# Kernel optimization log

Measured on AMD Instinct MI355X. Metric: run time of the kernel, lower is better.

## Reference

```python
import jax, jax.numpy as jnp
import numpy as np

EPS = 1e-8

def _gn1(x, w, b):
    # GroupNorm(num_groups=1): normalize each sample over (C, T), per-channel affine.
    mean = jnp.mean(x, axis=(1, 2), keepdims=True)
    var = jnp.mean((x - mean) ** 2, axis=(1, 2), keepdims=True)
    xn = (x - mean) * jax.lax.rsqrt(var + EPS)
    return xn * w[None, :, None] + b[None, :, None]

def _film(h, e, gw, gb, bw, bb):
    # gamma/beta: Linear -> ReLU (dropout is identity in eval), broadcast over time.
    gamma = jax.nn.relu(e @ gw.T + gb)  # [B, C]
    beta = jax.nn.relu(e @ bw.T + bb)   # [B, C]
    return gamma[:, :, None] * h + beta[:, :, None]

def setup_inputs() -> dict:
    key = jax.random.key(0)
    ks = jax.random.split(key, 16)
    B, C, T = 16, 256, 16000
    s = lambda k, shape, scale: jax.random.normal(k, shape, dtype=jnp.float32) * scale
    return {
        "x": s(ks[0], (B, C, T), 1.0),
        "cue": s(ks[1], (B, 512), 1.0),
        "gn_a_w": jnp.ones((C,), jnp.float32), "gn_a_b": jnp.zeros((C,), jnp.float32),
        "gn_n_w": jnp.ones((C,), jnp.float32), "gn_n_b": jnp.zeros((C,), jnp.float32),
        "f1g_w": s(ks[2], (C, 512), 0.04), "f1g_b": jnp.zeros((C,), jnp.float32),
        "f1b_w": s(ks[3], (C, 512), 0.04), "f1b_b": jnp.zeros((C,), jnp.float32),
        "ln1_w": jnp.ones((C,), jnp.float32), "ln1_b": jnp.zeros((C,), jnp.float32),
        "conv1_w": s(ks[4], (128, C), 0.06),
        "cds_w": s(ks[5], (256, 512), 0.04),
        "f2g_w": s(ks[6], (128, 256), 0.06), "f2g_b": jnp.zeros((128,), jnp.float32),
        "f2b_w": s(ks[7], (128, 256), 0.06), "f2b_b": jnp.zeros((128,), jnp.float32),
        "ln2_w": jnp.ones((128,), jnp.float32), "ln2_b": jnp.zeros((128,), jnp.float32),
        "conv2_w": s(ks[8], (256, 128), 0.08),
    }

def reference(x, cue, gn_a_w, gn_a_b, gn_n_w, gn_n_b, f1g_w, f1g_b, f1b_w, f1b_b,
              ln1_w, ln1_b, conv1_w, cds_w, f2g_w, f2g_b, f2b_w, f2b_b,
              ln2_w, ln2_b, conv2_w):
    x = _gn1(x, gn_a_w, gn_a_b)                 # norm_audio (GroupNorm(1, C))
    x = _gn1(x, gn_n_w, gn_n_b)                 # norm (GroupNorm(1, C))
    x = _film(x, cue, f1g_w, f1g_b, f1b_w, f1b_b) + x  # film1 + residual
    x = _gn1(x, ln1_w, ln1_b)                   # layer_norm1
    x = jnp.einsum('bct,oc->bot', x, conv1_w)   # 1x1 Conv1d, no bias -> [B,128,T]
    cue2 = jax.nn.relu(cue @ cds_w.T)           # cue_down_sample2 -> [B,256]
    x = _film(x, cue2, f2g_w, f2g_b, f2b_w, f2b_b) + x  # film2 + residual
    x = _gn1(x, ln2_w, ln2_b)                   # layer_norm2
    x = jnp.einsum('bct,oc->bot', x, conv2_w)   # 1x1 Conv1d -> [B,256,T]
    return x
```

## Files before the change

kernel.cpp:

```cpp
#include <hip/hip_runtime.h>
#include <hip/hip_bf16.h>
#include <hip/hip_fp16.h>

#define T_LEN   16000
#define NB      16
#define NTT     250
#define NTB     125
#define EPSV    1e-8f

typedef _Float16 f16x8 __attribute__((ext_vector_type(8)));
typedef float    f32x4 __attribute__((ext_vector_type(4)));

__device__ __forceinline__ ushort f2h(float f) {
    _Float16 h = (_Float16)f;
    return *(ushort*)&h;
}
__device__ __forceinline__ float f4c(const float4& v, int i) {
    return i == 0 ? v.x : i == 1 ? v.y : i == 2 ? v.z : v.w;
}
__device__ __forceinline__ void gld16(const ushort* g, ushort* l) {
    __builtin_amdgcn_global_load_lds(
        (const __attribute__((address_space(1))) uint*)g,
        (__attribute__((address_space(3))) uint*)l, 16, 0, 0);
}
__device__ __forceinline__ float waveRed64(float v) {
    #pragma unroll
    for (int m = 1; m <= 32; m <<= 1) v += __shfl_xor(v, m, 64);
    return v;
}
__device__ __forceinline__ float4 ntload4(const float* p) {
    f32x4 v = __builtin_nontemporal_load((const f32x4*)p);
    return make_float4(v[0], v[1], v[2], v[3]);
}

__global__ __launch_bounds__(256) void kP1F(
    const float* __restrict__ x, ushort* __restrict__ Xp,
    float* __restrict__ sp, float* __restrict__ qp,
    const float* __restrict__ cue,
    const float* __restrict__ f1g_w, const float* __restrict__ f1g_b,
    const float* __restrict__ f1b_w, const float* __restrict__ f1b_b,
    const float* __restrict__ cds_w,
    float* __restrict__ G1, float* __restrict__ B1, float* __restrict__ CUE2)
{
    const int bid = blockIdx.x;
    if (bid < 256) {
        const int c = bid;
        const int lane = threadIdx.x & 63, w = threadIdx.x >> 6;
        const float4 wg0 = *(const float4*)(f1g_w + c*512 + lane*8);
        const float4 wg1 = *(const float4*)(f1g_w + c*512 + lane*8 + 4);
        const float4 wb0 = *(const float4*)(f1b_w + c*512 + lane*8);
        const float4 wb1 = *(const float4*)(f1b_w + c*512 + lane*8 + 4);
        const float4 wc0 = *(const float4*)(cds_w + c*512 + lane*8);
        const float4 wc1 = *(const float4*)(cds_w + c*512 + lane*8 + 4);
        #pragma unroll
        for (int bb = 0; bb < 4; ++bb) {
            const int b = w*4 + bb;
            const float4 u0 = *(const float4*)(cue + b*512 + lane*8);
            const float4 u1 = *(const float4*)(cue + b*512 + lane*8 + 4);
            float g = 0.f, bt = 0.f, cv = 0.f;
            #pragma unroll
            for (int i = 0; i < 4; ++i) {
                g  = fmaf(f4c(u0,i), f4c(wg0,i), g);  g  = fmaf(f4c(u1,i), f4c(wg1,i), g);
                bt = fmaf(f4c(u0,i), f4c(wb0,i), bt); bt = fmaf(f4c(u1,i), f4c(wb1,i), bt);
                cv = fmaf(f4c(u0,i), f4c(wc0,i), cv); cv = fmaf(f4c(u1,i), f4c(wc1,i), cv);
            }
            g = waveRed64(g); bt = waveRed64(bt); cv = waveRed64(cv);
            if (lane == 0) {
                G1[b*256 + c]   = fmaxf(g + f1g_b[c], 0.f) + 1.f;
                B1[b*256 + c]   = fmaxf(bt + f1b_b[c], 0.f);
                CUE2[b*256 + c] = fmaxf(cv, 0.f);
            }
        }
        return;
    }

    const int pb = bid - 256;
    const int b = pb / NTT, tt = pb % NTT;
    const int t0 = tt * 64;
    const int tid = threadIdx.x;
    const int cq = tid >> 2, jq = tid & 3;
    __shared__ __align__(16) ushort Hs[256][68];

    #pragma unroll
    for (int cc = 0; cc < 4; ++cc) {
        const int c = cc*64 + cq;
        float s4 = 0.f, q4 = 0.f;
        #pragma unroll
        for (int i = 0; i < 4; ++i) {
            const int ts = (jq + i*4)*4;
            const float4 v = ntload4(x + ((size_t)(b*256 + c))*T_LEN + t0 + ts);
            s4 += v.x + v.y + v.z + v.w;
            q4 += v.x*v.x + v.y*v.y + v.z*v.z + v.w*v.w;
            const ushort h0 = f2h(v.x), h1 = f2h(v.y), h2 = f2h(v.z), h3 = f2h(v.w);
            uint2 pk;
            pk.x = (uint)h0 | ((uint)h1 << 16);
            pk.y = (uint)h2 | ((uint)h3 << 16);
            *(uint2*)&Hs[c][ts] = pk;
        }
        s4 += __shfl_xor(s4, 1, 4); s4 += __shfl_xor(s4, 2, 4);
        q4 += __shfl_xor(q4, 1, 4); q4 += __shfl_xor(q4, 2, 4);
        if (jq == 0) {
            sp[((size_t)b*NTT + tt)*256 + c] = s4;
            qp[((size_t)b*NTT + tt)*256 + c] = q4;
        }
    }
    __syncthreads();
    ushort* dst = Xp + ((size_t)(b*NTT + tt)*4)*4096;
    #pragma unroll
    for (int k = 0; k < 8; ++k) {
        const int d  = tid + k*256;
        const int kc = d >> 9, r = d & 511;
        const int t  = r >> 3, us = r & 7;
        const int u  = us ^ (t & 7);
        const int c0 = kc*64 + u*8;
        uint4 val;
        val.x = (uint)Hs[c0+0][t] | ((uint)Hs[c0+1][t] << 16);
        val.y = (uint)Hs[c0+2][t] | ((uint)Hs[c0+3][t] << 16);
        val.z = (uint)Hs[c0+4][t] | ((uint)Hs[c0+5][t] << 16);
        val.w = (uint)Hs[c0+6][t] | ((uint)Hs[c0+7][t] << 16);
        *(uint4*)(dst + (size_t)d*8) = val;
    }
}

__global__ __launch_bounds__(256) void kR_reduce(
    const float* __restrict__ sp, const float* __restrict__ qp,
    float* __restrict__ s1, float* __restrict__ q1)
{
    const int cg = blockIdx.x, b = blockIdx.y;
    const int ci = threadIdx.x & 31, ig = threadIdx.x >> 5;
    const int c = cg*32 + ci;
    float s = 0.f, q = 0.f;
    for (int i = ig; i < NTT; i += 8) {
        s += sp[((size_t)b*NTT + i)*256 + c];
        q += qp[((size_t)b*NTT + i)*256 + c];
    }
    __shared__ float rs[8][32], rq[8][32];
    rs[ig][ci] = s; rq[ig][ci] = q;
    __syncthreads();
    if (threadIdx.x < 32) {
        float ss = 0.f, qq = 0.f;
        #pragma unroll
        for (int g = 0; g < 8; ++g) { ss += rs[g][threadIdx.x]; qq += rq[g][threadIdx.x]; }
        s1[b*256 + cg*32 + threadIdx.x] = ss;
        q1[b*256 + cg*32 + threadIdx.x] = qq;
    }
}

__device__ __forceinline__ float blockSum256(float v, float* red)
{
    #pragma unroll
    for (int off = 32; off; off >>= 1) v += __shfl_down(v, off, 64);
    __syncthreads();
    if ((threadIdx.x & 63) == 0) red[threadIdx.x >> 6] = v;
    __syncthreads();
    return red[0] + red[1] + red[2] + red[3];
}

__global__ __launch_bounds__(256) void kBM_stats(
    const float* __restrict__ s1, const float* __restrict__ q1,
    const float* __restrict__ gn_a_w, const float* __restrict__ gn_a_b,
    const float* __restrict__ gn_n_w, const float* __restrict__ gn_n_b,
    const float* __restrict__ G1, const float* __restrict__ B1,
    const float* __restrict__ ln1_w, const float* __restrict__ ln1_b,
    float* __restrict__ a4o, float* __restrict__ d4o)
{
    const int b = blockIdx.x;
    const int c = threadIdx.x;
    __shared__ float red[4];

    const float sc = s1[b*256 + c];
    const float qc = q1[b*256 + c];

    const float Ninv = 1.f / (256.f * 16000.f);
    const float Tf = 16000.f;

    float S  = blockSum256(sc, red);
    float Q  = blockSum256(qc, red);
    float mu1 = S * Ninv;
    float var1 = Q * Ninv - mu1 * mu1;
    float r1 = rsqrtf(var1 + EPSV);
    float a1 = gn_a_w[c] * r1;
    float d1 = gn_a_b[c] - mu1 * r1 * gn_a_w[c];

    float S2 = blockSum256(a1*sc + Tf*d1, red);
    float Q2 = blockSum256(a1*a1*qc + 2.f*a1*d1*sc + Tf*d1*d1, red);
    float mu2 = S2 * Ninv;
    float var2 = Q2 * Ninv - mu2 * mu2;
    float r2 = rsqrtf(var2 + EPSV);
    float wn = gn_n_w[c];
    float a2 = wn * r2 * a1;
    float d2 = wn * r2 * (d1 - mu2) + gn_n_b[c];

    const float g1 = G1[b*256 + c];
    const float b1 = B1[b*256 + c];
    float a3 = g1 * a2;
    float d3 = g1 * d2 + b1;

    float S3 = blockSum256(a3*sc + Tf*d3, red);
    float Q3 = blockSum256(a3*a3*qc + 2.f*a3*d3*sc + Tf*d3*d3, red);
    float mu3 = S3 * Ninv;
    float var3 = Q3 * Ninv - mu3 * mu3;
    float r3 = rsqrtf(var3 + EPSV);
    float w1 = ln1_w[c];
    a4o[b*256 + c] = w1 * r3 * a3;
    d4o[b*256 + c] = w1 * r3 * (d3 - mu3) + ln1_b[c];
}

__global__ __launch_bounds__(256) void kM2(
    const float* __restrict__ CUE2,
    const float* __restrict__ f2g_w, const float* __restrict__ f2g_b,
    const float* __restrict__ f2b_w, const float* __restrict__ f2b_b,
    const float* __restrict__ conv1_w,
    const float* __restrict__ a4, const float* __restrict__ d4,
    float* __restrict__ G2, float* __restrict__ E, ushort* __restrict__ Msf)
{
    const int og = blockIdx.x, b = blockIdx.y;
    const int tid = threadIdx.x;
    __shared__ float sc2[256], sa4[256], sd4[256], sg2[16];
    sc2[tid] = CUE2[b*256 + tid];
    sa4[tid] = a4[b*256 + tid];
    sd4[tid] = d4[b*256 + tid];
    __syncthreads();

    const int oi = tid >> 4, l16 = tid & 15;
    const int o = og*16 + oi;
    float g = 0.f, bt = 0.f, ed = 0.f;
    #pragma unroll
    for (int q = 0; q < 4; ++q) {
        const int k0 = l16*16 + q*4;
        const float4 a  = *(const float4*)(f2g_w  + o*256 + k0);
        const float4 bb = *(const float4*)(f2b_w  + o*256 + k0);
        const float4 c  = *(const float4*)(conv1_w + o*256 + k0);
        const float4 u  = *(const float4*)(&sc2[k0]);
        const float4 dd = *(const float4*)(&sd4[k0]);
        #pragma unroll
        for (int i = 0; i < 4; ++i) {
            g  = fmaf(f4c(u,i),  f4c(a,i),  g);
            bt = fmaf(f4c(u,i),  f4c(bb,i), bt);
            ed = fmaf(f4c(dd,i), f4c(c,i),  ed);
        }
    }
    #pragma unroll
    for (int m = 1; m <= 8; m <<= 1) {
        g  += __shfl_xor(g, m, 16);
        bt += __shfl_xor(bt, m, 16);
        ed += __shfl_xor(ed, m, 16);
    }
    if (l16 == 0) {
        const float G2v = fmaxf(g + f2g_b[o], 0.f) + 1.f;
        const float B2v = fmaxf(bt + f2b_b[o], 0.f);
        G2[b*128 + o] = G2v;
        E[b*128 + o]  = G2v * ed + B2v;
        sg2[oi] = G2v;
    }
    __syncthreads();
    const float av = sa4[tid];
    #pragma unroll
    for (int i = 0; i < 16; ++i) {
        const int oo = og*16 + i;
        Msf[((size_t)b*128 + oo)*256 + tid] = f2h(sg2[i] * conv1_w[oo*256 + tid] * av);
    }
}

__global__ __launch_bounds__(256) void kC_gemm(
    const ushort* __restrict__ Xp, const ushort* __restrict__ Msf,
    const float* __restrict__ E,
    float* __restrict__ q2p)
{
    const int tb = blockIdx.x, b = blockIdx.y;
    const int tid = threadIdx.x, lane = tid & 63, w = tid >> 6;
    const int wo = w >> 1, wt = w & 1;
    const int sub = lane >> 4, li = lane & 15;
    const int o0 = wo * 64;
    __shared__ __align__(16) ushort Bs[32768];
    __shared__ float sQp[2][128];

    const ushort* src = Xp + ((size_t)(b*NTT + 2*tb)*4)*4096;
    const ushort* mp  = Msf + (size_t)b*128*256;

    f32x4 acc[4][4];
    #pragma unroll
    for (int i = 0; i < 4; ++i)
        #pragma unroll
        for (int jx = 0; jx < 4; ++jx) acc[i][jx] = (f32x4){0.f,0.f,0.f,0.f};

    #pragma unroll
    for (int m = 0; m < 16; ++m) {
        const int off = m*2048 + w*512;
        gld16(src + off + lane*8, &Bs[off]);
    }
    __syncthreads();

    #pragma unroll
    for (int ks = 0; ks < 8; ++ks) {
        const int kc = ks >> 1;
        const int uo = (ks & 1)*4 + sub;
        f16x8 xf[4];
        #pragma unroll
        for (int ft = 0; ft < 4; ++ft) {
            const int tl = ft*16 + li;
            xf[ft] = *(const f16x8*)&Bs[(wt*4 + kc)*4096 + tl*64 + (uo ^ (tl & 7))*8];
        }
        const int k8 = kc*64 + (ks & 1)*32 + 8*sub;
        #pragma unroll
        for (int fo = 0; fo < 4; ++fo) {
            const f16x8 mf = *(const f16x8*)(mp + (size_t)(o0 + fo*16 + li)*256 + k8);
            #pragma unroll
            for (int ft = 0; ft < 4; ++ft)
                acc[ft][fo] = __builtin_amdgcn_mfma_f32_16x16x32_f16(xf[ft], mf, acc[ft][fo], 0, 0, 0);
        }
    }

    #pragma unroll
    for (int fo = 0; fo < 4; ++fo) {
        const int o = o0 + fo*16 + li;
        const float ev = E[b*128 + o];
        float qv = 0.f;
        #pragma unroll
        for (int ft = 0; ft < 4; ++ft)
            #pragma unroll
            for (int r = 0; r < 4; ++r) {
                const float z = acc[ft][fo][r] + ev;
                qv += z*z;
            }
        qv += __shfl_xor(qv, 16, 64); qv += __shfl_xor(qv, 32, 64);
        if (sub == 0) sQp[wt][o] = qv;
    }
    __syncthreads();
    if (tid < 128)
        q2p[((size_t)b*NTB + tb)*128 + tid] = sQp[0][tid] + sQp[1][tid];
}

__global__ __launch_bounds__(256) void kD2_buildF(
    const float* __restrict__ q2p,
    const float* __restrict__ ln2_w, const float* __restrict__ ln2_b,
    const float* __restrict__ Ev,
    const float* __restrict__ a4, const float* __restrict__ G2,
    const float* __restrict__ s1,
    const float* __restrict__ conv1_w, const float* __restrict__ conv2_w,
    ushort* __restrict__ Fsf, float* __restrict__ h)
{
    const int b = blockIdx.y, pg = blockIdx.x;
    const int tid = threadIdx.x;
    __shared__ float Qs[32][128];
    __shared__ float sA2[128], sAE[128], sAS[256];
    __shared__ float rS[2], rQ[2];

    sAS[tid] = a4[b*256 + tid] * s1[b*256 + tid];
    __syncthreads();

    float s2v = 0.f, qq = 0.f;
    if (tid < 128) {
        float dot = 0.f;
        #pragma unroll 4
        for (int c4 = 0; c4 < 64; ++c4) {
            const float4 cw = *(const float4*)(conv1_w + tid*256 + c4*4);
            const float4 as = *(const float4*)(&sAS[c4*4]);
            dot = fmaf(cw.x, as.x, dot); dot = fmaf(cw.y, as.y, dot);
            dot = fmaf(cw.z, as.z, dot); dot = fmaf(cw.w, as.w, dot);
        }
        s2v = G2[b*128 + tid] * dot + 16000.f * Ev[b*128 + tid];
        for (int tb = 0; tb < NTB; ++tb)
            qq += q2p[((size_t)b*NTB + tb)*128 + tid];
        float S = s2v, Q = qq;
        #pragma unroll
        for (int off = 32; off; off >>= 1) {
            S += __shfl_down(S, off, 64);
            Q += __shfl_down(Q, off, 64);
        }
        if ((tid & 63) == 0) { rS[tid >> 6] = S; rQ[tid >> 6] = Q; }
    }
    __syncthreads();
    const float N2inv = 1.f / (128.f * 16000.f);
    const float mu  = (rS[0] + rS[1]) * N2inv;
    const float var = (rQ[0] + rQ[1]) * N2inv - mu * mu;
    const float r = rsqrtf(var + EPSV);
    if (tid < 128) {
        const float a2v = ln2_w[tid] * r;
        const float d2v = ln2_b[tid] - mu * ln2_w[tid] * r;
        sA2[tid] = a2v;
        sAE[tid] = a2v * Ev[b*128 + tid] + d2v;
    }
    __syncthreads();

    #pragma unroll
    for (int k = 0; k < 16; ++k) {
        const int idx = tid + k*256;
        const int p = idx >> 7, o = idx & 127;
        Qs[p][o] = conv2_w[(pg*32 + p)*128 + o] * sA2[o] * G2[b*128 + o];
    }
    __syncthreads();
    float acc[32];
    #pragma unroll
    for (int p = 0; p < 32; ++p) acc[p] = 0.f;
    for (int o = 0; o < 128; ++o) {
        const float mv = conv1_w[o*256 + tid];
        #pragma unroll
        for (int p = 0; p < 32; ++p) acc[p] = fmaf(Qs[p][o], mv, acc[p]);
    }
    const float a = a4[b*256 + tid];
    #pragma unroll
    for (int p = 0; p < 32; ++p) {
        const size_t idx = ((size_t)b*256 + pg*32 + p)*256 + tid;
        Fsf[idx] = f2h(acc[p] * a);
    }
    if (tid < 32) {
        const int p = pg*32 + tid;
        float hv = 0.f;
        for (int o = 0; o < 128; ++o)
            hv += conv2_w[p*128 + o] * sAE[o];
        h[b*256 + p] = hv;
    }
}

__global__ __launch_bounds__(256) void kE_gemm(
    const ushort* __restrict__ Xp, const ushort* __restrict__ Fsf,
    const float* __restrict__ h, float* __restrict__ out)
{
    const int tt = blockIdx.x;
    const int b = blockIdx.y >> 1;
    const int o_base = (blockIdx.y & 1) * 128;
    const int tid = threadIdx.x, lane = tid & 63, w = tid >> 6;
    const int sub = lane >> 4, li = lane & 15;
    const int o0 = o_base + w * 32, t0 = tt * 64;
    __shared__ __align__(16) ushort Bs[16384];

    const ushort* src = Xp + ((size_t)(b*NTT + tt)*4)*4096;
    const ushort* fp  = Fsf + (size_t)b*65536;

    f32x4 acc[4][2];
    #pragma unroll
    for (int i = 0; i < 4; ++i)
        #pragma unroll
        for (int jx = 0; jx < 2; ++jx) acc[i][jx] = (f32x4){0.f,0.f,0.f,0.f};

    #pragma unroll
    for (int m = 0; m < 8; ++m) {
        const int off = m*2048 + w*512;
        gld16(src + off + lane*8, &Bs[off]);
    }
    __syncthreads();

    #pragma unroll
    for (int ks = 0; ks < 8; ++ks) {
        const int kc = ks >> 1;
        const int uo = (ks & 1)*4 + sub;
        f16x8 xf[4];
        #pragma unroll
        for (int ft = 0; ft < 4; ++ft) {
            const int tl = ft*16 + li;
            xf[ft] = *(const f16x8*)&Bs[kc*4096 + tl*64 + (uo ^ (tl & 7))*8];
        }
        const int k8 = kc*64 + (ks & 1)*32 + 8*sub;
        #pragma unroll
        for (int fo = 0; fo < 2; ++fo) {
            const f16x8 ff = *(const f16x8*)(fp + (size_t)(o0 + fo*16 + li)*256 + k8);
            #pragma unroll
            for (int ft = 0; ft < 4; ++ft)
                acc[ft][fo] = __builtin_amdgcn_mfma_f32_16x16x32_f16(xf[ft], ff, acc[ft][fo], 0, 0, 0);
        }
    }

    #pragma unroll
    for (int fo = 0; fo < 2; ++fo) {
        const int o = o0 + fo*16 + li;
        const float hv = h[b*256 + o];
        float* obase = out + ((size_t)(b*256 + o))*T_LEN + t0;
        #pragma unroll
        for (int ft = 0; ft < 4; ++ft) {
            f32x4 v;
            v[0] = acc[ft][fo][0] + hv;
            v[1] = acc[ft][fo][1] + hv;
            v[2] = acc[ft][fo][2] + hv;
            v[3] = acc[ft][fo][3] + hv;
            __builtin_nontemporal_store(v, (f32x4*)(obase + ft*16 + sub*4));
        }
    }
}

extern "C" void kernel_launch(void* const* d_in, const int* in_sizes, int n_in,
                              void* d_out, int out_size, void* d_ws, size_t ws_size,
                              hipStream_t stream)
{
    const float* x       = (const float*)d_in[0];
    const float* cue     = (const float*)d_in[1];
    const float* gn_a_w  = (const float*)d_in[2];
    const float* gn_a_b  = (const float*)d_in[3];
    const float* gn_n_w  = (const float*)d_in[4];
    const float* gn_n_b  = (const float*)d_in[5];
    const float* f1g_w   = (const float*)d_in[6];
    const float* f1g_b   = (const float*)d_in[7];
    const float* f1b_w   = (const float*)d_in[8];
    const float* f1b_b   = (const float*)d_in[9];
    const float* ln1_w   = (const float*)d_in[10];
    const float* ln1_b   = (const float*)d_in[11];
    const float* conv1_w = (const float*)d_in[12];
    const float* cds_w   = (const float*)d_in[13];
    const float* f2g_w   = (const float*)d_in[14];
    const float* f2g_b   = (const float*)d_in[15];
    const float* f2b_w   = (const float*)d_in[16];
    const float* f2b_b   = (const float*)d_in[17];
    const float* ln2_w   = (const float*)d_in[18];
    const float* ln2_b   = (const float*)d_in[19];
    const float* conv2_w = (const float*)d_in[20];
    float* out = (float*)d_out;

    float* ws = (float*)d_ws;
    float*  sp   = ws;
    float*  qp   = ws + 1024000;
    float*  G1   = ws + 2048000;
    float*  B1   = ws + 2052096;
    float*  CUE2 = ws + 2056192;
    float*  G2   = ws + 2060288;
    float*  a4   = ws + 2062336;
    float*  d4   = ws + 2066432;
    float*  E    = ws + 2070528;
    float*  h    = ws + 2072576;
    float*  s1   = ws + 2076672;
    float*  q1   = ws + 2080768;
    float*  q2p  = ws + 2084864;
    ushort* Msf  = (ushort*)(ws + 2340864);
    ushort* Fsf  = (ushort*)(ws + 2603008);
    ushort* Xp   = (ushort*)(ws + 3127296);

    kP1F<<<256 + NTT*NB, 256, 0, stream>>>(x, Xp, sp, qp,
        cue, f1g_w, f1g_b, f1b_w, f1b_b, cds_w, G1, B1, CUE2);

    kR_reduce<<<dim3(8, NB), 256, 0, stream>>>(sp, qp, s1, q1);

    kBM_stats<<<NB, 256, 0, stream>>>(s1, q1, gn_a_w, gn_a_b, gn_n_w, gn_n_b,
                                      G1, B1, ln1_w, ln1_b, a4, d4);

    kM2<<<dim3(8, NB), 256, 0, stream>>>(CUE2, f2g_w, f2g_b, f2b_w, f2b_b,
                                         conv1_w, a4, d4, G2, E, Msf);

    kC_gemm<<<dim3(NTB, NB), 256, 0, stream>>>(Xp, Msf, E, q2p);

    kD2_buildF<<<dim3(8, NB), 256, 0, stream>>>(q2p, ln2_w, ln2_b, E,
                                                a4, G2, s1, conv1_w, conv2_w,
                                                Fsf, h);

    kE_gemm<<<dim3(NTT, NB*2), 256, 0, stream>>>(Xp, Fsf, h, out);
}
```

Measured before the change: 306.5 us.

## Fuse partial-stat reduction and GroupNorm stats into P1 via last-block atomic counters

Removes the separate kR_reduce and kBM_stats launches. Each time-tile block of kP1F increments a per-batch atomic counter, and the last block for each batch waits for the FiLM blocks to finish through a global counter. That block then reduces the partial sums and computes the normalization coefficients inline. This saves two kernel launches and their tail gaps, but adds a memset, a spin-wait, and a serial 250-step reduction done by a single block per batch.

```diff
diff --git a/kernel.cpp b/kernel.cpp
--- a/kernel.cpp
+++ b/kernel.cpp
@@ -31,6 +31,16 @@
 __device__ __forceinline__ float4 ntload4(const float* p) {
     f32x4 v = __builtin_nontemporal_load((const f32x4*)p);
     return make_float4(v[0], v[1], v[2], v[3]);
+}
+
+__device__ __forceinline__ float blockSum256(float v, float* red)
+{
+    #pragma unroll
+    for (int off = 32; off; off >>= 1) v += __shfl_down(v, off, 64);
+    __syncthreads();
+    if ((threadIdx.x & 63) == 0) red[threadIdx.x >> 6] = v;
+    __syncthreads();
+    return red[0] + red[1] + red[2] + red[3];
 }
 
 __global__ __launch_bounds__(256) void kP1F(
@@ -40,12 +50,19 @@
     const float* __restrict__ f1g_w, const float* __restrict__ f1g_b,
     const float* __restrict__ f1b_w, const float* __restrict__ f1b_b,
     const float* __restrict__ cds_w,
-    float* __restrict__ G1, float* __restrict__ B1, float* __restrict__ CUE2)
+    float* __restrict__ G1, float* __restrict__ B1, float* __restrict__ CUE2,
+    int* __restrict__ cnt,
+    const float* __restrict__ gn_a_w, const float* __restrict__ gn_a_b,
+    const float* __restrict__ gn_n_w, const float* __restrict__ gn_n_b,
+    const float* __restrict__ ln1_w,  const float* __restrict__ ln1_b,
+    float* __restrict__ s1, float* __restrict__ a4o, float* __restrict__ d4o)
 {
     const int bid = blockIdx.x;
+    const int tid = threadIdx.x;
+
     if (bid < 256) {
         const int c = bid;
-        const int lane = threadIdx.x & 63, w = threadIdx.x >> 6;
+        const int lane = tid & 63, w = tid >> 6;
         const float4 wg0 = *(const float4*)(f1g_w + c*512 + lane*8);
         const float4 wg1 = *(const float4*)(f1g_w + c*512 + lane*8 + 4);
         const float4 wb0 = *(const float4*)(f1b_w + c*512 + lane*8);
@@ -71,15 +88,19 @@
                 CUE2[b*256 + c] = fmaxf(cv, 0.f);
             }
         }
+        __threadfence();
+        __syncthreads();
+        if (tid == 0) atomicAdd(&cnt[0], 1);
         return;
     }
 
     const int pb = bid - 256;
     const int b = pb / NTT, tt = pb % NTT;
     const int t0 = tt * 64;
-    const int tid = threadIdx.x;
     const int cq = tid >> 2, jq = tid & 3;
     __shared__ __align__(16) ushort Hs[256][68];
+    __shared__ float red[4];
+    __shared__ int isw;
 
     #pragma unroll
     for (int cc = 0; cc < 4; ++cc) {
@@ -120,56 +141,29 @@
         val.w = (uint)Hs[c0+6][t] | ((uint)Hs[c0+7][t] << 16);
         *(uint4*)(dst + (size_t)d*8) = val;
     }
-}
-
-__global__ __launch_bounds__(256) void kR_reduce(
-    const float* __restrict__ sp, const float* __restrict__ qp,
-    float* __restrict__ s1, float* __restrict__ q1)
-{
-    const int cg = blockIdx.x, b = blockIdx.y;
-    const int ci = threadIdx.x & 31, ig = threadIdx.x >> 5;
-    const int c = cg*32 + ci;
-    float s = 0.f, q = 0.f;
-    for (int i = ig; i < NTT; i += 8) {
-        s += sp[((size_t)b*NTT + i)*256 + c];
-        q += qp[((size_t)b*NTT + i)*256 + c];
-    }
-    __shared__ float rs[8][32], rq[8][32];
-    rs[ig][ci] = s; rq[ig][ci] = q;
-    __syncthreads();
-    if (threadIdx.x < 32) {
-        float ss = 0.f, qq = 0.f;
-        #pragma unroll
-        for (int g = 0; g < 8; ++g) { ss += rs[g][threadIdx.x]; qq += rq[g][threadIdx.x]; }
-        s1[b*256 + cg*32 + threadIdx.x] = ss;
-        q1[b*256 + cg*32 + threadIdx.x] = qq;
-    }
-}
-
-__device__ __forceinline__ float blockSum256(float v, float* red)
-{
-    #pragma unroll
-    for (int off = 32; off; off >>= 1) v += __shfl_down(v, off, 64);
-    __syncthreads();
-    if ((threadIdx.x & 63) == 0) red[threadIdx.x >> 6] = v;
-    __syncthreads();
-    return red[0] + red[1] + red[2] + red[3];
-}
-
-__global__ __launch_bounds__(256) void kBM_stats(
-    const float* __restrict__ s1, const float* __restrict__ q1,
-    const float* __restrict__ gn_a_w, const float* __restrict__ gn_a_b,
-    const float* __restrict__ gn_n_w, const float* __restrict__ gn_n_b,
-    const float* __restrict__ G1, const float* __restrict__ B1,
-    const float* __restrict__ ln1_w, const float* __restrict__ ln1_b,
-    float* __restrict__ a4o, float* __restrict__ d4o)
-{
-    const int b = blockIdx.x;
-    const int c = threadIdx.x;
-    __shared__ float red[4];
-
-    const float sc = s1[b*256 + c];
-    const float qc = q1[b*256 + c];
+
+    __threadfence();
+    __syncthreads();
+    if (tid == 0) {
+        const int old = atomicAdd(&cnt[1 + b], 1);
+        isw = (old == NTT - 1) ? 1 : 0;
+    }
+    __syncthreads();
+    if (!isw) return;
+
+    if (tid == 0) {
+        while (atomicAdd(&cnt[0], 0) < 256) { }
+    }
+    __syncthreads();
+    __threadfence();
+
+    const int c = tid;
+    float sc = 0.f, qc = 0.f;
+    for (int i = 0; i < NTT; ++i) {
+        sc += sp[((size_t)b*NTT + i)*256 + c];
+        qc += qp[((size_t)b*NTT + i)*256 + c];
+    }
+    s1[b*256 + c] = sc;
 
     const float Ninv = 1.f / (256.f * 16000.f);
     const float Tf = 16000.f;
@@ -517,19 +511,18 @@
     float*  E    = ws + 2070528;
     float*  h    = ws + 2072576;
     float*  s1   = ws + 2076672;
-    float*  q1   = ws + 2080768;
-    float*  q2p  = ws + 2084864;
-    ushort* Msf  = (ushort*)(ws + 2340864);
-    ushort* Fsf  = (ushort*)(ws + 2603008);
-    ushort* Xp   = (ushort*)(ws + 3127296);
+    float*  q2p  = ws + 2080768;
+    int*    cnt  = (int*)(ws + 2336768);
+    ushort* Msf  = (ushort*)(ws + 2336800);
+    ushort* Fsf  = (ushort*)(ws + 2598944);
+    ushort* Xp   = (ushort*)(ws + 3123232);
+
+    hipMemsetAsync(cnt, 0, 128, stream);
 
     kP1F<<<256 + NTT*NB, 256, 0, stream>>>(x, Xp, sp, qp,
-        cue, f1g_w, f1g_b, f1b_w, f1b_b, cds_w, G1, B1, CUE2);
-
-    kR_reduce<<<dim3(8, NB), 256, 0, stream>>>(sp, qp, s1, q1);
-
-    kBM_stats<<<NB, 256, 0, stream>>>(s1, q1, gn_a_w, gn_a_b, gn_n_w, gn_n_b,
-                                      G1, B1, ln1_w, ln1_b, a4, d4);
+        cue, f1g_w, f1g_b, f1b_w, f1b_b, cds_w, G1, B1, CUE2,
+        cnt, gn_a_w, gn_a_b, gn_n_w, gn_n_b, ln1_w, ln1_b,
+        s1, a4, d4);
 
     kM2<<<dim3(8, NB), 256, 0, stream>>>(CUE2, f2g_w, f2g_b, f2b_w, f2b_b,
                                          conv1_w, a4, d4, G2, E, Msf);
```

Measured after the change: 1.108 ms. 262% more time.

## Fuse stats kernel into kM2 and double-buffer two time tiles in kE_gemm

Applied to the files above, without the earlier changes.

Merges the per-batch GroupNorm stats kernel into the FiLM2/Msf builder, so each of the 8 blocks per batch recomputes the stats redundantly and one launch plus the d4 round trip go away. kE_gemm now processes two 64-sample time tiles per block: the F weight fragments are loaded into registers once, and the second X tile is prefetched into a second LDS buffer while the first is computed. This halves the grid and reuses weight loads, at the cost of more registers and LDS per block, which may lower occupancy.

```diff
diff --git a/kernel.cpp b/kernel.cpp
--- a/kernel.cpp
+++ b/kernel.cpp
@@ -31,6 +31,16 @@
 __device__ __forceinline__ float4 ntload4(const float* p) {
     f32x4 v = __builtin_nontemporal_load((const f32x4*)p);
     return make_float4(v[0], v[1], v[2], v[3]);
+}
+
+__device__ __forceinline__ float blockSum256(float v, float* red)
+{
+    #pragma unroll
+    for (int off = 32; off; off >>= 1) v += __shfl_down(v, off, 64);
+    __syncthreads();
+    if ((threadIdx.x & 63) == 0) red[threadIdx.x >> 6] = v;
+    __syncthreads();
+    return red[0] + red[1] + red[2] + red[3];
 }
 
 __global__ __launch_bounds__(256) void kP1F(
@@ -146,27 +156,23 @@
     }
 }
 
-__device__ __forceinline__ float blockSum256(float v, float* red)
-{
-    #pragma unroll
-    for (int off = 32; off; off >>= 1) v += __shfl_down(v, off, 64);
-    __syncthreads();
-    if ((threadIdx.x & 63) == 0) red[threadIdx.x >> 6] = v;
-    __syncthreads();
-    return red[0] + red[1] + red[2] + red[3];
-}
-
-__global__ __launch_bounds__(256) void kBM_stats(
+__global__ __launch_bounds__(256) void kM2F(
     const float* __restrict__ s1, const float* __restrict__ q1,
     const float* __restrict__ gn_a_w, const float* __restrict__ gn_a_b,
     const float* __restrict__ gn_n_w, const float* __restrict__ gn_n_b,
     const float* __restrict__ G1, const float* __restrict__ B1,
     const float* __restrict__ ln1_w, const float* __restrict__ ln1_b,
-    float* __restrict__ a4o, float* __restrict__ d4o)
-{
-    const int b = blockIdx.x;
+    const float* __restrict__ CUE2,
+    const float* __restrict__ f2g_w, const float* __restrict__ f2g_b,
+    const float* __restrict__ f2b_w, const float* __restrict__ f2b_b,
+    const float* __restrict__ conv1_w,
+    float* __restrict__ a4o, float* __restrict__ G2,
+    float* __restrict__ E, ushort* __restrict__ Msf)
+{
+    const int og = blockIdx.x, b = blockIdx.y;
     const int c = threadIdx.x;
     __shared__ float red[4];
+    __shared__ float sc2[256], sa4[256], sd4[256], sg2[16];
 
     const float sc = s1[b*256 + c];
     const float qc = q1[b*256 + c];
@@ -191,10 +197,10 @@
     float a2 = wn * r2 * a1;
     float d2 = wn * r2 * (d1 - mu2) + gn_n_b[c];
 
-    const float g1 = G1[b*256 + c];
-    const float b1 = B1[b*256 + c];
-    float a3 = g1 * a2;
-    float d3 = g1 * d2 + b1;
+    const float g1v = G1[b*256 + c];
+    const float b1v = B1[b*256 + c];
+    float a3 = g1v * a2;
+    float d3 = g1v * d2 + b1v;
 
     float S3 = blockSum256(a3*sc + Tf*d3, red);
     float Q3 = blockSum256(a3*a3*qc + 2.f*a3*d3*sc + Tf*d3*d3, red);
@@ -202,27 +208,15 @@
     float var3 = Q3 * Ninv - mu3 * mu3;
     float r3 = rsqrtf(var3 + EPSV);
     float w1 = ln1_w[c];
-    a4o[b*256 + c] = w1 * r3 * a3;
-    d4o[b*256 + c] = w1 * r3 * (d3 - mu3) + ln1_b[c];
-}
-
-__global__ __launch_bounds__(256) void kM2(
-    const float* __restrict__ CUE2,
-    const float* __restrict__ f2g_w, const float* __restrict__ f2g_b,
-    const float* __restrict__ f2b_w, const float* __restrict__ f2b_b,
-    const float* __restrict__ conv1_w,
-    const float* __restrict__ a4, const float* __restrict__ d4,
-    float* __restrict__ G2, float* __restrict__ E, ushort* __restrict__ Msf)
-{
-    const int og = blockIdx.x, b = blockIdx.y;
-    const int tid = threadIdx.x;
-    __shared__ float sc2[256], sa4[256], sd4[256], sg2[16];
-    sc2[tid] = CUE2[b*256 + tid];
-    sa4[tid] = a4[b*256 + tid];
-    sd4[tid] = d4[b*256 + tid];
-    __syncthreads();
-
-    const int oi = tid >> 4, l16 = tid & 15;
+    const float a4v = w1 * r3 * a3;
+    const float d4v = w1 * r3 * (d3 - mu3) + ln1_b[c];
+    sa4[c] = a4v;
+    sd4[c] = d4v;
+    if (og == 0) a4o[b*256 + c] = a4v;
+    sc2[c] = CUE2[b*256 + c];
+    __syncthreads();
+
+    const int oi = c >> 4, l16 = c & 15;
     const int o = og*16 + oi;
     float g = 0.f, bt = 0.f, ed = 0.f;
     #pragma unroll
@@ -230,14 +224,14 @@
         const int k0 = l16*16 + q*4;
         const float4 a  = *(const float4*)(f2g_w  + o*256 + k0);
         const float4 bb = *(const float4*)(f2b_w  + o*256 + k0);
-        const float4 c  = *(const float4*)(conv1_w + o*256 + k0);
+        const float4 cc = *(const float4*)(conv1_w + o*256 + k0);
         const float4 u  = *(const float4*)(&sc2[k0]);
         const float4 dd = *(const float4*)(&sd4[k0]);
         #pragma unroll
         for (int i = 0; i < 4; ++i) {
             g  = fmaf(f4c(u,i),  f4c(a,i),  g);
             bt = fmaf(f4c(u,i),  f4c(bb,i), bt);
-            ed = fmaf(f4c(dd,i), f4c(c,i),  ed);
+            ed = fmaf(f4c(dd,i), f4c(cc,i), ed);
         }
     }
     #pragma unroll
@@ -254,11 +248,11 @@
         sg2[oi] = G2v;
     }
     __syncthreads();
-    const float av = sa4[tid];
+    const float av = sa4[c];
     #pragma unroll
     for (int i = 0; i < 16; ++i) {
         const int oo = og*16 + i;
-        Msf[((size_t)b*128 + oo)*256 + tid] = f2h(sg2[i] * conv1_w[oo*256 + tid] * av);
+        Msf[((size_t)b*128 + oo)*256 + c] = f2h(sg2[i] * conv1_w[oo*256 + c] * av);
     }
 }
 
@@ -417,64 +411,87 @@
     const ushort* __restrict__ Xp, const ushort* __restrict__ Fsf,
     const float* __restrict__ h, float* __restrict__ out)
 {
-    const int tt = blockIdx.x;
+    const int txp = blockIdx.x;
     const int b = blockIdx.y >> 1;
     const int o_base = (blockIdx.y & 1) * 128;
     const int tid = threadIdx.x, lane = tid & 63, w = tid >> 6;
     const int sub = lane >> 4, li = lane & 15;
-    const int o0 = o_base + w * 32, t0 = tt * 64;
-    __shared__ __align__(16) ushort Bs[16384];
-
-    const ushort* src = Xp + ((size_t)(b*NTT + tt)*4)*4096;
-    const ushort* fp  = Fsf + (size_t)b*65536;
-
-    f32x4 acc[4][2];
-    #pragma unroll
-    for (int i = 0; i < 4; ++i)
-        #pragma unroll
-        for (int jx = 0; jx < 2; ++jx) acc[i][jx] = (f32x4){0.f,0.f,0.f,0.f};
+    const int o0 = o_base + w * 32;
+    __shared__ __align__(16) ushort Bs[2][16384];
+
+    const ushort* fp = Fsf + (size_t)b*65536;
+
+    f16x8 ff[8][2];
+    #pragma unroll
+    for (int ks = 0; ks < 8; ++ks) {
+        const int k8 = (ks >> 1)*64 + (ks & 1)*32 + 8*sub;
+        #pragma unroll
+        for (int fo = 0; fo < 2; ++fo)
+            ff[ks][fo] = *(const f16x8*)(fp + (size_t)(o0 + fo*16 + li)*256 + k8);
+    }
+    float hv[2];
+    #pragma unroll
+    for (int fo = 0; fo < 2; ++fo)
+        hv[fo] = h[b*256 + o0 + fo*16 + li];
+
+    const ushort* src0 = Xp + ((size_t)(b*NTT + 2*txp)*4)*4096;
 
     #pragma unroll
     for (int m = 0; m < 8; ++m) {
         const int off = m*2048 + w*512;
-        gld16(src + off + lane*8, &Bs[off]);
-    }
-    __syncthreads();
-
-    #pragma unroll
-    for (int ks = 0; ks < 8; ++ks) {
-        const int kc = ks >> 1;
-        const int uo = (ks & 1)*4 + sub;
-        f16x8 xf[4];
-        #pragma unroll
-        for (int ft = 0; ft < 4; ++ft) {
-            const int tl = ft*16 + li;
-            xf[ft] = *(const f16x8*)&Bs[kc*4096 + tl*64 + (uo ^ (tl & 7))*8];
-        }
-        const int k8 = kc*64 + (ks & 1)*32 + 8*sub;
+        gld16(src0 + off + lane*8, &Bs[0][off]);
+    }
+    __syncthreads();
+
+    #pragma unroll
+    for (int tile = 0; tile < 2; ++tile) {
+        if (tile == 0) {
+            const ushort* src1 = src0 + 16384;
+            #pragma unroll
+            for (int m = 0; m < 8; ++m) {
+                const int off = m*2048 + w*512;
+                gld16(src1 + off + lane*8, &Bs[1][off]);
+            }
+        }
+        f32x4 acc[4][2];
+        #pragma unroll
+        for (int i = 0; i < 4; ++i)
+            #pragma unroll
+            for (int jx = 0; jx < 2; ++jx) acc[i][jx] = (f32x4){0.f,0.f,0.f,0.f};
+
+        #pragma unroll
+        for (int ks = 0; ks < 8; ++ks) {
+            const int kc = ks >> 1;
+            const int uo = (ks & 1)*4 + sub;
+            f16x8 xf[4];
+            #pragma unroll
+            for (int ft = 0; ft < 4; ++ft) {
+                const int tl = ft*16 + li;
+                xf[ft] = *(const f16x8*)&Bs[tile][kc*4096 + tl*64 + (uo ^ (tl & 7))*8];
+            }
+            #pragma unroll
+            for (int fo = 0; fo < 2; ++fo)
+                #pragma unroll
+                for (int ft = 0; ft < 4; ++ft)
+                    acc[ft][fo] = __builtin_amdgcn_mfma_f32_16x16x32_f16(xf[ft], ff[ks][fo], acc[ft][fo], 0, 0, 0);
+        }
+
+        const int t0 = (2*txp + tile)*64;
         #pragma unroll
         for (int fo = 0; fo < 2; ++fo) {
-            const f16x8 ff = *(const f16x8*)(fp + (size_t)(o0 + fo*16 + li)*256 + k8);
-            #pragma unroll
-            for (int ft = 0; ft < 4; ++ft)
-                acc[ft][fo] = __builtin_amdgcn_mfma_f32_16x16x32_f16(xf[ft], ff, acc[ft][fo], 0, 0, 0);
-        }
-    }
-
-    #pragma unroll
-    for (int fo = 0; fo < 2; ++fo) {
-        const int o = o0 + fo*16 + li;
-        const float hv = h[b*256 + o];
-        float* obase = out + ((size_t)(b*256 + o))*T_LEN + t0;
-        #pragma unroll
-        for (int ft = 0; ft < 4; ++ft) {
-            f32x4 v;
-            v[0] = acc[ft][fo][0] + hv;
-            v[1] = acc[ft][fo][1] + hv;
-            v[2] = acc[ft][fo][2] + hv;
-            v[3] = acc[ft][fo][3] + hv;
-            __builtin_nontemporal_store(v, (f32x4*)(obase + ft*16 + sub*4));
-        }
+            const int o = o0 + fo*16 + li;
+            float* obase = out + ((size_t)(b*256 + o))*T_LEN + t0;
+            #pragma unroll
+            for (int ft = 0; ft < 4; ++ft) {
+                f32x4 v;
+                v[0] = acc[ft][fo][0] + hv[fo];
+                v[1] = acc[ft][fo][1] + hv[fo];
+                v[2] = acc[ft][fo][2] + hv[fo];
+                v[3] = acc[ft][fo][3] + hv[fo];
+                __builtin_nontemporal_store(v, (f32x4*)(obase + ft*16 + sub*4));
+            }
+        }
+        if (tile == 0) __syncthreads();
     }
 }
 
@@ -513,26 +530,24 @@
     float*  CUE2 = ws + 2056192;
     float*  G2   = ws + 2060288;
     float*  a4   = ws + 2062336;
-    float*  d4   = ws + 2066432;
-    float*  E    = ws + 2070528;
-    float*  h    = ws + 2072576;
-    float*  s1   = ws + 2076672;
-    float*  q1   = ws + 2080768;
-    float*  q2p  = ws + 2084864;
-    ushort* Msf  = (ushort*)(ws + 2340864);
-    ushort* Fsf  = (ushort*)(ws + 2603008);
-    ushort* Xp   = (ushort*)(ws + 3127296);
+    float*  E    = ws + 2066432;
+    float*  h    = ws + 2068480;
+    float*  s1   = ws + 2072576;
+    float*  q1   = ws + 2076672;
+    float*  q2p  = ws + 2080768;
+    ushort* Msf  = (ushort*)(ws + 2336768);
+    ushort* Fsf  = (ushort*)(ws + 2598912);
+    ushort* Xp   = (ushort*)(ws + 3123200);
 
     kP1F<<<256 + NTT*NB, 256, 0, stream>>>(x, Xp, sp, qp,
         cue, f1g_w, f1g_b, f1b_w, f1b_b, cds_w, G1, B1, CUE2);
 
     kR_reduce<<<dim3(8, NB), 256, 0, stream>>>(sp, qp, s1, q1);
 
-    kBM_stats<<<NB, 256, 0, stream>>>(s1, q1, gn_a_w, gn_a_b, gn_n_w, gn_n_b,
-                                      G1, B1, ln1_w, ln1_b, a4, d4);
-
-    kM2<<<dim3(8, NB), 256, 0, stream>>>(CUE2, f2g_w, f2g_b, f2b_w, f2b_b,
-                                         conv1_w, a4, d4, G2, E, Msf);
+    kM2F<<<dim3(8, NB), 256, 0, stream>>>(s1, q1,
+        gn_a_w, gn_a_b, gn_n_w, gn_n_b, G1, B1, ln1_w, ln1_b,
+        CUE2, f2g_w, f2g_b, f2b_w, f2b_b, conv1_w,
+        a4, G2, E, Msf);
 
     kC_gemm<<<dim3(NTB, NB), 256, 0, stream>>>(Xp, Msf, E, q2p);
 
@@ -540,5 +555,5 @@
                                                 a4, G2, s1, conv1_w, conv2_w,
                                                 Fsf, h);
 
-    kE_gemm<<<dim3(NTT, NB*2), 256, 0, stream>>>(Xp, Fsf, h, out);
-}
+    kE_gemm<<<dim3(NTB, NB*2), 256, 0, stream>>>(Xp, Fsf, h, out);
+}
```

New measurement: 293.2 us. 4.3% less time.
